# Performance work log

Hardware: AMD Instinct MI355X
Metric: run time of the kernel (lower is better)

Reference implementation:

```python
import jax, jax.numpy as jnp
import numpy as np

SIZE = 256  # matrix dimension n; input vector length = n*(n-1)/2
BATCH = 512

# strictly-lower indices in the same row-major (i, j<i) order as the module's l_indices
_ROWS, _COLS = np.tril_indices(SIZE, k=-1)


def setup_inputs() -> dict:
    key = jax.random.key(0)
    m = SIZE * (SIZE - 1) // 2
    # z entries are partial-correlation-like values, must lie in (-1, 1)
    vec = jax.random.uniform(key, (BATCH, m), dtype=jnp.float32, minval=-0.99, maxval=0.99)
    return {"vec": vec}


def reference(vec):
    B = vec.shape[0]
    n = SIZE
    # scatter vector into strictly-lower triangle: (B, n, n)
    z = jnp.zeros((B, n, n), dtype=vec.dtype).at[:, _ROWS, _COLS].set(vec)
    signs = jnp.sign(z)
    signs = jnp.where(signs == 0, jnp.asarray(1.0, vec.dtype), signs)
    z2 = z * z

    row_idx = jnp.arange(n)  # (n,)

    def step(rowsum, inp):
        # rowsum: (B, n) running sum of x_squared over already-built columns, per row
        j, z2_col = inp  # z2_col: (B, n) = z^2[:, :, j]
        base = z2_col * (1.0 - rowsum)           # lower entries (rows > j)
        col = jnp.where(row_idx[None, :] == j, jnp.asarray(1.0, vec.dtype),
                        jnp.where(row_idx[None, :] < j, jnp.asarray(0.0, vec.dtype), base))
        return rowsum + col, col

    z2_cols = jnp.moveaxis(z2, -1, 0)  # (n_col, B, n_row)
    _, x2_cols = jax.lax.scan(step, jnp.zeros((B, n), dtype=vec.dtype),
                              (jnp.arange(n), z2_cols))
    # x2_cols: (n_col, B, n_row) -> (B, n_row, n_col)
    x2 = jnp.moveaxis(x2_cols, 0, -1)
    return jnp.sqrt(x2) * signs
```

## Files before the change

### kernel.cpp

```cpp
#include <hip/hip_runtime.h>


#define SIZE 256
#define BATCH 512
#define M (SIZE * (SIZE - 1) / 2)
#define TOTAL (BATCH * M)
#define NWAVES (BATCH * SIZE)
#define NBLOCKS (NWAVES / 4)

typedef float f4u __attribute__((ext_vector_type(4), aligned(4)));
typedef float f4a __attribute__((ext_vector_type(4), aligned(16)));

template <int CTRL, int ROW_MASK>
__device__ __forceinline__ float scan_mul(float p) {
    int sh = __builtin_amdgcn_update_dpp(
        __builtin_bit_cast(int, 1.0f),
        __builtin_bit_cast(int, p),
        CTRL, ROW_MASK, 0xF, false);
    return p * __builtin_bit_cast(float, sh);
}

__device__ __forceinline__ float excl_shift_one(float p) {
    int r = __builtin_amdgcn_update_dpp(
        __builtin_bit_cast(int, 1.0f),
        __builtin_bit_cast(int, p),
        0x138 , 0xF, 0xF, false);
    return __builtin_bit_cast(float, r);
}

__global__ __launch_bounds__(256) void chol_from_z_kernel(
    const float* __restrict__ vec, float* __restrict__ out) {
    const int lane = threadIdx.x & 63;
    const int wib = __builtin_amdgcn_readfirstlane((int)threadIdx.x >> 6);

    const int bid = (int)blockIdx.x;
    const int sbid = (bid & 7) * (NBLOCKS / 8) + (bid >> 3);

    const int wave = sbid * 4 + wib;
    const int b = wave >> 8;
    const int i = wave & 255;
    const int row_off = b * M + ((i * (i - 1)) >> 1);
    const float* __restrict__ s = vec + row_off;
    float* __restrict__ dst = out + ((size_t)wave << 8);
    const int j0 = lane << 2;

    const int ja = (j0 < i) ? j0 : 0;
    const int maxidx = (TOTAL - 1) - row_off;
    f4u zv;
    if (maxidx >= 255) {
        zv = *(const f4u*)(s + ja);
    } else {
        zv.x = s[ja]; zv.y = s[ja + 1]; zv.z = s[ja + 2];
        zv.w = (ja + 3 <= maxidx) ? s[ja + 3] : 0.f;
    }

    const float z0 = (j0     < i) ? zv.x : 0.f;
    const float z1 = (j0 + 1 < i) ? zv.y : 0.f;
    const float z2 = (j0 + 2 < i) ? zv.z : 0.f;
    const float z3 = (j0 + 3 < i) ? zv.w : 0.f;

    const float t0 = 1.f - z0 * z0;
    const float t1 = 1.f - z1 * z1;
    const float t2 = 1.f - z2 * z2;
    const float t3 = 1.f - z3 * z3;

    float p = (t0 * t1) * (t2 * t3);

    p = scan_mul<0x111, 0xF>(p);
    p = scan_mul<0x112, 0xF>(p);
    p = scan_mul<0x114, 0xF>(p);
    p = scan_mul<0x118, 0xF>(p);
    if (i >= 64)  p = scan_mul<0x142, 0xA>(p);
    if (i >= 128) p = scan_mul<0x143, 0xC>(p);

    float run = excl_shift_one(p);

    f4a o;
    o.x = (j0     == i) ? 1.f : z0 * __builtin_amdgcn_sqrtf(run); run *= t0;
    o.y = (j0 + 1 == i) ? 1.f : z1 * __builtin_amdgcn_sqrtf(run); run *= t1;
    o.z = (j0 + 2 == i) ? 1.f : z2 * __builtin_amdgcn_sqrtf(run); run *= t2;
    o.w = (j0 + 3 == i) ? 1.f : z3 * __builtin_amdgcn_sqrtf(run);

    *(f4a*)(dst + j0) = o;
}

extern "C" void kernel_launch(void* const* d_in, const int* in_sizes, int n_in,
                              void* d_out, int out_size, void* d_ws, size_t ws_size,
                              hipStream_t stream) {
    const float* vec = (const float*)d_in[0];
    float* out = (float*)d_out;
    chol_from_z_kernel<<<NBLOCKS, 256, 0, stream>>>(vec, out);
}
```

Measured before the change: 180.8 us.

## Make waves persistent over 16 batches with software-prefetched row loads

Launches a fixed 8192 waves instead of one wave per (batch,row). Each wave loops over 16 batch entries with a stride of 32 batches and prefetches the next row's input while computing and storing the current one. This drops the XCD-aware block swizzle and adds a min-blocks launch bound. The aim is to hide load latency and amortise wave launch, at the cost of fewer concurrent waves and longer serial chains per wave. Tail-bound handling now applies only to the last wave's final iteration.

```diff
diff --git a/kernel.cpp b/kernel.cpp
--- a/kernel.cpp
+++ b/kernel.cpp
@@ -5,8 +5,11 @@
 #define BATCH 512
 #define M (SIZE * (SIZE - 1) / 2)
 #define TOTAL (BATCH * M)
-#define NWAVES (BATCH * SIZE)
+#define NWAVES 8192
 #define NBLOCKS (NWAVES / 4)
+#define NITER (BATCH * SIZE / NWAVES)
+#define STEP (32 * M)
+#define DSTEP ((size_t)NWAVES * SIZE)
 
 typedef float f4u __attribute__((ext_vector_type(4), aligned(4)));
 typedef float f4a __attribute__((ext_vector_type(4), aligned(16)));
@@ -28,60 +31,69 @@
     return __builtin_bit_cast(float, r);
 }
 
-__global__ __launch_bounds__(256) void chol_from_z_kernel(
+__global__ __launch_bounds__(256, 4) void chol_from_z_kernel(
     const float* __restrict__ vec, float* __restrict__ out) {
     const int lane = threadIdx.x & 63;
     const int wib = __builtin_amdgcn_readfirstlane((int)threadIdx.x >> 6);
-
-    const int bid = (int)blockIdx.x;
-    const int sbid = (bid & 7) * (NBLOCKS / 8) + (bid >> 3);
-
-    const int wave = sbid * 4 + wib;
-    const int b = wave >> 8;
-    const int i = wave & 255;
-    const int row_off = b * M + ((i * (i - 1)) >> 1);
-    const float* __restrict__ s = vec + row_off;
-    float* __restrict__ dst = out + ((size_t)wave << 8);
+    const int wv = (int)blockIdx.x * 4 + wib;
+    const int i = wv & 255;
     const int j0 = lane << 2;
 
-    const int ja = (j0 < i) ? j0 : 0;
-    const int maxidx = (TOTAL - 1) - row_off;
-    f4u zv;
-    if (maxidx >= 255) {
-        zv = *(const f4u*)(s + ja);
-    } else {
-        zv.x = s[ja]; zv.y = s[ja + 1]; zv.z = s[ja + 2];
-        zv.w = (ja + 3 <= maxidx) ? s[ja + 3] : 0.f;
+    const bool m0 = (j0     < i), m1 = (j0 + 1 < i);
+    const bool m2 = (j0 + 2 < i), m3 = (j0 + 3 < i);
+    const bool d0 = (j0     == i), d1 = (j0 + 1 == i);
+    const bool d2 = (j0 + 2 == i), d3 = (j0 + 3 == i);
+    const bool last_wave = (wv == NWAVES - 1);
+
+    const float* sp = vec + (wv >> 8) * M + ((i * (i - 1)) >> 1) + j0;
+    float* dst = out + ((size_t)wv << 8) + j0;
+
+    f4u cur = *(const f4u*)sp;
+
+#pragma unroll
+    for (int t = 0; t < NITER; ++t) {
+        f4u nxt = cur;
+        if (t + 1 < NITER) {
+            sp += STEP;
+            if (!(last_wave && t + 1 == NITER - 1)) {
+                nxt = *(const f4u*)sp;
+            } else {
+                nxt.x = sp[0]; nxt.y = sp[1]; nxt.z = sp[2];
+                nxt.w = (j0 + 3 < 255) ? sp[3] : 0.f;
+            }
+        }
+
+        const float z0 = m0 ? cur.x : 0.f;
+        const float z1 = m1 ? cur.y : 0.f;
+        const float z2 = m2 ? cur.z : 0.f;
+        const float z3 = m3 ? cur.w : 0.f;
+
+        const float t0 = 1.f - z0 * z0;
+        const float t1 = 1.f - z1 * z1;
+        const float t2 = 1.f - z2 * z2;
+        const float t3 = 1.f - z3 * z3;
+
+        float p = (t0 * t1) * (t2 * t3);
+
+        p = scan_mul<0x111, 0xF>(p);
+        p = scan_mul<0x112, 0xF>(p);
+        p = scan_mul<0x114, 0xF>(p);
+        p = scan_mul<0x118, 0xF>(p);
+        if (i >= 64)  p = scan_mul<0x142, 0xA>(p);
+        if (i >= 128) p = scan_mul<0x143, 0xC>(p);
+
+        float run = excl_shift_one(p);
+
+        f4a o;
+        o.x = d0 ? 1.f : z0 * __builtin_amdgcn_sqrtf(run); run *= t0;
+        o.y = d1 ? 1.f : z1 * __builtin_amdgcn_sqrtf(run); run *= t1;
+        o.z = d2 ? 1.f : z2 * __builtin_amdgcn_sqrtf(run); run *= t2;
+        o.w = d3 ? 1.f : z3 * __builtin_amdgcn_sqrtf(run);
+
+        *(f4a*)dst = o;
+        dst += DSTEP;
+        cur = nxt;
     }
-
-    const float z0 = (j0     < i) ? zv.x : 0.f;
-    const float z1 = (j0 + 1 < i) ? zv.y : 0.f;
-    const float z2 = (j0 + 2 < i) ? zv.z : 0.f;
-    const float z3 = (j0 + 3 < i) ? zv.w : 0.f;
-
-    const float t0 = 1.f - z0 * z0;
-    const float t1 = 1.f - z1 * z1;
-    const float t2 = 1.f - z2 * z2;
-    const float t3 = 1.f - z3 * z3;
-
-    float p = (t0 * t1) * (t2 * t3);
-
-    p = scan_mul<0x111, 0xF>(p);
-    p = scan_mul<0x112, 0xF>(p);
-    p = scan_mul<0x114, 0xF>(p);
-    p = scan_mul<0x118, 0xF>(p);
-    if (i >= 64)  p = scan_mul<0x142, 0xA>(p);
-    if (i >= 128) p = scan_mul<0x143, 0xC>(p);
-
-    float run = excl_shift_one(p);
-
-    f4a o;
-    o.x = (j0     == i) ? 1.f : z0 * __builtin_amdgcn_sqrtf(run); run *= t0;
-    o.y = (j0 + 1 == i) ? 1.f : z1 * __builtin_amdgcn_sqrtf(run); run *= t1;
-    o.z = (j0 + 2 == i) ? 1.f : z2 * __builtin_amdgcn_sqrtf(run); run *= t2;
-    o.w = (j0 + 3 == i) ? 1.f : z3 * __builtin_amdgcn_sqrtf(run);
-
-    *(f4a*)(dst + j0) = o;
 }
 
 extern "C" void kernel_launch(void* const* d_in, const int* in_sizes, int n_in,
```

Result: no change. 183.7 us (+1.6%).
